# Performance work log

Measured on AMD Instinct MI355X. Metric: run time of the kernel, lower is better.

Reference implementation:

```python
import jax, jax.numpy as jnp
import numpy as np

B = 4; IMG = 32; P = 2; C_IN = 3; H_DIM = 384; DEPTH = 8
GS = IMG // P; L = GS * GS
NSTATE = 16; KDIR = 4; DIN = 384; RANK = 24; MH = int(H_DIM * 4.0)
BOT = 128; NCLS = 1000; TFREQ = 256


def _silu(x):
    return x * jax.nn.sigmoid(x)


def _rms(x, w, eps=1e-6):
    return x * jax.lax.rsqrt(jnp.mean(x * x, -1, keepdims=True) + eps) * w


def _ln(x, w, b, eps=1e-5):
    mu = jnp.mean(x, -1, keepdims=True)
    v = jnp.mean((x - mu) ** 2, -1, keepdims=True)
    return (x - mu) * jax.lax.rsqrt(v + eps) * w + b


def _ln_na(x, eps=1e-6):
    mu = jnp.mean(x, -1, keepdims=True)
    v = jnp.mean((x - mu) ** 2, -1, keepdims=True)
    return (x - mu) * jax.lax.rsqrt(v + eps)


def _mod(x, shift, scale):
    return x * (1.0 + scale[:, None, :]) + shift[:, None, :]


def _ss2d(xin, in_w, conv_w, conv_b, xproj_w, dt_w, dt_b, A_logs, Ds, onorm_w, onorm_b, outp_w):
    Bb = xin.shape[0]
    z = xin @ in_w.T  # (B,L,DIN)
    z2d = z.reshape(Bb, GS, GS, DIN).transpose(0, 3, 1, 2)  # (B,DIN,H,W)
    z2d = jax.lax.conv_general_dilated(z2d, conv_w, (1, 1), 'SAME',
        feature_group_count=DIN, dimension_numbers=('NCHW', 'OIHW', 'NCHW'))
    z2d = _silu(z2d + conv_b[None, :, None, None])
    # cross_scan -> (B,K,DIN,L): row-major, reversed, col-major, reversed col-major
    s1 = z2d.reshape(Bb, DIN, L)
    s3 = z2d.transpose(0, 1, 3, 2).reshape(Bb, DIN, L)
    xs = jnp.stack([s1, s1[..., ::-1], s3, s3[..., ::-1]], axis=1)
    x_dbl = jnp.einsum('bkdl,kod->bkol', xs, xproj_w)
    dtr = x_dbl[:, :, :RANK]
    Bssm = x_dbl[:, :, RANK:RANK + NSTATE]   # (B,K,N,L)
    Cssm = x_dbl[:, :, RANK + NSTATE:]       # (B,K,N,L)
    dt = jnp.einsum('bkrl,kdr->bkdl', dtr, dt_w)
    dt = jax.nn.softplus(dt + dt_b[None, :, :, None])
    A = -jnp.exp(A_logs)                     # (K,DIN,N)
    dA = jnp.exp(jnp.einsum('bkdl,kdn->bkldn', dt, A))
    dBu = jnp.einsum('bkdl,bknl->bkldn', dt * xs, Bssm)
    def comb(e1, e2):
        a1, b1 = e1
        a2, b2 = e2
        return a1 * a2, a2 * b1 + b2
    _, hs = jax.lax.associative_scan(comb, (dA, dBu), axis=2)  # h over token axis
    ys = jnp.einsum('bkldn,bknl->bkdl', hs, Cssm) + Ds[None, :, :, None] * xs
    # cross_merge: undo each direction's reorder and sum
    m1 = ys[:, 0]
    m2 = ys[:, 1][..., ::-1]
    m3 = ys[:, 2].reshape(Bb, DIN, GS, GS).swapaxes(2, 3).reshape(Bb, DIN, L)
    m4 = ys[:, 3][..., ::-1].reshape(Bb, DIN, GS, GS).swapaxes(2, 3).reshape(Bb, DIN, L)
    out = (m1 + m2 + m3 + m4).transpose(0, 2, 1)  # (B,L,DIN)
    out = _ln(out, onorm_w, onorm_b)
    return out @ outp_w.T


def _forward(x, t, y, t_w1, t_b1, t_w2, t_b2, y_table, pe_w1, pe_w2, pe_b2, pos_embed,
             adaln_w, adaln_b, n1_w, n2_w, in_w, conv_w, conv_b, xproj_w, dt_w, dt_b,
             A_logs, Ds, onorm_w, onorm_b, outp_w, mlp_w1, mlp_b1, mlp_w2, mlp_b2,
             f_adaln_w, f_adaln_b, f_lin_w, f_lin_b):
    # timestep embedding (DiT TimestepEmbedder, freq dim 256)
    half = TFREQ // 2
    freqs = jnp.exp(-jnp.log(10000.0) * jnp.arange(half, dtype=jnp.float32) / half)
    ang = t[:, None] * freqs[None]
    temb = jnp.concatenate([jnp.cos(ang), jnp.sin(ang)], axis=-1)
    temb = _silu(temb @ t_w1.T + t_b1) @ t_w2.T + t_b2
    c = temb + y_table[y]  # (B,H_DIM)
    # bottleneck patch embed: patchify -> bottleneck linear -> hidden linear
    xp = x.reshape(B, C_IN, GS, P, GS, P).transpose(0, 2, 4, 1, 3, 5).reshape(B, L, C_IN * P * P)
    h = (xp @ pe_w1.T) @ pe_w2.T + pe_b2
    h = h + pos_embed
    for i in range(DEPTH):
        mod = _silu(c) @ adaln_w[i].T + adaln_b[i]
        sh1, sc1, g1, sh2, sc2, g2 = jnp.split(mod, 6, axis=-1)
        h = h + g1[:, None] * _ss2d(_mod(_rms(h, n1_w[i]), sh1, sc1),
            in_w[i], conv_w[i], conv_b[i], xproj_w[i], dt_w[i], dt_b[i],
            A_logs[i], Ds[i], onorm_w[i], onorm_b[i], outp_w[i])
        u = _mod(_rms(h, n2_w[i]), sh2, sc2)
        u12 = u @ mlp_w1[i].T + mlp_b1[i]
        u1, u2 = jnp.split(u12, 2, axis=-1)
        h = h + g2[:, None] * ((_silu(u1) * u2) @ mlp_w2[i].T + mlp_b2[i])
    modf = _silu(c) @ f_adaln_w.T + f_adaln_b
    shf, scf = jnp.split(modf, 2, axis=-1)
    h = _mod(_ln_na(h), shf, scf)
    out = h @ f_lin_w.T + f_lin_b  # (B,L,P*P*C_IN)
    out = out.reshape(B, GS, GS, P, P, C_IN)
    out = jnp.einsum('nhwpqc->nchpwq', out)
    return out.reshape(B, C_IN, IMG, IMG)


def _sincos_1d(dim, pos):
    omega = 1.0 / (10000.0 ** (np.arange(dim // 2, dtype=np.float64) / (dim / 2.0)))
    out = pos.reshape(-1)[:, None] * omega[None, :]
    return np.concatenate([np.sin(out), np.cos(out)], axis=1)


def _pos_embed_np(dim, gs):
    g = np.stack(np.meshgrid(np.arange(gs, dtype=np.float64), np.arange(gs, dtype=np.float64)), axis=0)
    return np.concatenate([_sincos_1d(dim // 2, g[0]), _sincos_1d(dim // 2, g[1])], axis=1).astype(np.float32)


def setup_inputs():
    key = jax.random.key(0)
    ks = iter(jax.random.split(key, 64))
    nrm = lambda shape, s=0.02: jax.random.normal(next(ks), shape, jnp.float32) * s
    d = {}
    d['x'] = jax.random.normal(next(ks), (B, C_IN, IMG, IMG), jnp.float32)
    d['t'] = jax.random.uniform(next(ks), (B,), jnp.float32) * 1000.0
    d['y'] = jax.random.randint(next(ks), (B,), 0, NCLS)
    d['t_w1'] = nrm((H_DIM, TFREQ)); d['t_b1'] = jnp.zeros((H_DIM,), jnp.float32)
    d['t_w2'] = nrm((H_DIM, H_DIM)); d['t_b2'] = jnp.zeros((H_DIM,), jnp.float32)
    d['y_table'] = nrm((NCLS, H_DIM))
    d['pe_w1'] = nrm((BOT, C_IN * P * P), 0.1)
    d['pe_w2'] = nrm((H_DIM, BOT), 0.1); d['pe_b2'] = jnp.zeros((H_DIM,), jnp.float32)
    d['pos_embed'] = jnp.asarray(_pos_embed_np(H_DIM, GS))[None]
    d['adaln_w'] = nrm((DEPTH, 6 * H_DIM, H_DIM)); d['adaln_b'] = jnp.zeros((DEPTH, 6 * H_DIM), jnp.float32)
    d['n1_w'] = jnp.ones((DEPTH, H_DIM), jnp.float32); d['n2_w'] = jnp.ones((DEPTH, H_DIM), jnp.float32)
    d['in_w'] = nrm((DEPTH, DIN, H_DIM), 0.05)
    d['conv_w'] = nrm((DEPTH, DIN, 1, 3, 3), 0.1); d['conv_b'] = jnp.zeros((DEPTH, DIN), jnp.float32)
    d['xproj_w'] = nrm((DEPTH, KDIR, RANK + 2 * NSTATE, DIN), 0.05)
    d['dt_w'] = nrm((DEPTH, KDIR, DIN, RANK), 0.1)
    d['dt_b'] = nrm((DEPTH, KDIR, DIN), 0.5)
    d['A_logs'] = jnp.tile(jnp.log(jnp.arange(1, NSTATE + 1, dtype=jnp.float32))[None, None, None, :], (DEPTH, KDIR, DIN, 1))
    d['Ds'] = jnp.ones((DEPTH, KDIR, DIN), jnp.float32)
    d['onorm_w'] = jnp.ones((DEPTH, DIN), jnp.float32); d['onorm_b'] = jnp.zeros((DEPTH, DIN), jnp.float32)
    d['outp_w'] = nrm((DEPTH, H_DIM, DIN), 0.05)
    d['mlp_w1'] = nrm((DEPTH, 2 * MH, H_DIM)); d['mlp_b1'] = jnp.zeros((DEPTH, 2 * MH), jnp.float32)
    d['mlp_w2'] = nrm((DEPTH, H_DIM, MH)); d['mlp_b2'] = jnp.zeros((DEPTH, H_DIM), jnp.float32)
    d['f_adaln_w'] = nrm((2 * H_DIM, H_DIM)); d['f_adaln_b'] = jnp.zeros((2 * H_DIM,), jnp.float32)
    d['f_lin_w'] = nrm((P * P * C_IN, H_DIM)); d['f_lin_b'] = jnp.zeros((P * P * C_IN,), jnp.float32)
    return d


def reference(x, t, y, t_w1, t_b1, t_w2, t_b2, y_table, pe_w1, pe_w2, pe_b2, pos_embed,
              adaln_w, adaln_b, n1_w, n2_w, in_w, conv_w, conv_b, xproj_w, dt_w, dt_b,
              A_logs, Ds, onorm_w, onorm_b, outp_w, mlp_w1, mlp_b1, mlp_w2, mlp_b2,
              f_adaln_w, f_adaln_b, f_lin_w, f_lin_b):
    return _forward(x, t, y, t_w1, t_b1, t_w2, t_b2, y_table, pe_w1, pe_w2, pe_b2, pos_embed,
                    adaln_w, adaln_b, n1_w, n2_w, in_w, conv_w, conv_b, xproj_w, dt_w, dt_b,
                    A_logs, Ds, onorm_w, onorm_b, outp_w, mlp_w1, mlp_b1, mlp_w2, mlp_b2,
                    f_adaln_w, f_adaln_b, f_lin_w, f_lin_b)
```

## Files before the change

### kernel.cpp

```cpp
#include <hip/hip_runtime.h>
#include <hip/hip_bf16.h>
#include <math.h>


#define DEV __device__ __forceinline__

typedef __bf16 bf16_t;
typedef __attribute__((ext_vector_type(8))) __bf16 bf16x8;
typedef __attribute__((ext_vector_type(4))) float f32x4;
typedef __attribute__((ext_vector_type(2))) _Float16 h2;

DEV float siluf(float x){ return x / (1.f + __expf(-x)); }
DEV float softplusf(float x){ return fmaxf(x, 0.f) + __logf(1.f + __expf(-fabsf(x))); }

DEV int perm_idx(int k, int l){
  switch(k & 3){
    case 0: return l;
    case 1: return 255 - l;
    case 2: return ((l & 15) << 4) | (l >> 4);
    default: { int r = 255 - l; return ((r & 15) << 4) | (r >> 4); }
  }
}

DEV void cvt_one(int idx, const float* inw, const float* outw, const float* w1,
                 const float* w2, const float* xp, bf16_t* dst){
  const float* src; int off;
  if (idx < 147456){ src = inw;  off = idx; }
  else if (idx < 294912){ src = outw; off = idx - 147456; }
  else if (idx < 1474560){
    int o = idx - 294912;
    int rowc = o / 384, col = o - rowc*384;
    int q = rowc >> 5, tt = rowc & 31;
    int srow = (tt < 16) ? (q*16 + tt) : (1536 + q*16 + (tt - 16));
    src = w1; off = srow*384 + col;
  }
  else if (idx < 2064384){ src = w2; off = idx - 1474560; }
  else { src = xp; off = idx - 2064384; }
  float4 v = *(const float4*)(src + off);
  union { bf16_t h[4]; uint2 u; } cv;
  cv.h[0] = (bf16_t)v.x; cv.h[1] = (bf16_t)v.y; cv.h[2] = (bf16_t)v.z; cv.h[3] = (bf16_t)v.w;
  *(uint2*)(dst + idx) = cv.u;
}

__global__ void k_cvt_layer(const float* __restrict__ inw, const float* __restrict__ outw,
                            const float* __restrict__ w1, const float* __restrict__ w2,
                            const float* __restrict__ xp, bf16_t* __restrict__ dst){
  int idx = (blockIdx.x*256 + threadIdx.x)*4;
  cvt_one(idx, inw, outw, w1, w2, xp, dst);
}

__global__ void k_cvt_all(const float* __restrict__ inw, const float* __restrict__ outw,
                          const float* __restrict__ w1, const float* __restrict__ w2,
                          const float* __restrict__ xp, bf16_t* __restrict__ dst){
  int layer = blockIdx.x / 2100;
  int within = blockIdx.x % 2100;
  int idx = (within*256 + threadIdx.x)*4;
  cvt_one(idx, inw + (size_t)layer*147456, outw + (size_t)layer*147456,
          w1 + (size_t)layer*1179648, w2 + (size_t)layer*589824,
          xp + (size_t)layer*86016, dst + (size_t)layer*2150400);
}

__global__ void k_cond(const float* __restrict__ t, const int* __restrict__ y,
                       const float* __restrict__ tw1, const float* __restrict__ tb1,
                       const float* __restrict__ tw2, const float* __restrict__ tb2,
                       const float* __restrict__ ytab, float* __restrict__ sc){
  int b = blockIdx.x; int o = threadIdx.x;
  __shared__ float temb[256]; __shared__ float h1[384];
  float tv = t[b];
  if (o < 128){
    float f = __expf(-logf(10000.f) * (float)o / 128.f);
    float a = tv * f;
    temb[o] = cosf(a); temb[128 + o] = sinf(a);
  }
  __syncthreads();
  float acc = tb1[o];
  for (int j = 0; j < 256; j++) acc += temb[j] * tw1[(size_t)o*256 + j];
  h1[o] = siluf(acc);
  __syncthreads();
  float acc2 = tb2[o];
  for (int j = 0; j < 384; j++) acc2 += h1[j] * tw2[(size_t)o*384 + j];
  float c = acc2 + ytab[(size_t)y[b]*384 + o];
  sc[b*384 + o] = siluf(c);
}

__global__ void k_patch(const float* __restrict__ x, const float* __restrict__ pw1,
                        const float* __restrict__ pw2, const float* __restrict__ pb2,
                        const float* __restrict__ pos, float* __restrict__ h){
  int bl = blockIdx.x; int b = bl >> 8; int l = bl & 255;
  int gh = l >> 4, gw = l & 15;
  __shared__ float xp[12]; __shared__ float tmp[128];
  int tid = threadIdx.x;
  if (tid < 12){
    int ci = tid >> 2, ph = (tid >> 1) & 1, pw = tid & 1;
    xp[tid] = x[((size_t)(b*3 + ci)*32 + gh*2 + ph)*32 + gw*2 + pw];
  }
  __syncthreads();
  if (tid < 128){
    float a = 0.f;
    #pragma unroll
    for (int k = 0; k < 12; k++) a += xp[k] * pw1[tid*12 + k];
    tmp[tid] = a;
  }
  __syncthreads();
  float a = pb2[tid];
  for (int j = 0; j < 128; j++) a += tmp[j] * pw2[(size_t)tid*128 + j];
  h[(size_t)(b*256 + l)*384 + tid] = a + pos[(size_t)l*384 + tid];
}

__global__ void k_lin_small(const float* __restrict__ sc, const float* __restrict__ W,
                            const float* __restrict__ bias, float* __restrict__ out, int N){
  int idx = blockIdx.x * blockDim.x + threadIdx.x;
  if (idx >= 4*N) return;
  int b = idx / N, o = idx % N;
  const float4* cp = (const float4*)(sc + b*384);
  const float4* wp = (const float4*)(W + (size_t)o*384);
  float a = bias[o];
  #pragma unroll 4
  for (int k = 0; k < 96; k++){
    float4 c4 = cp[k], w4 = wp[k];
    a += c4.x*w4.x + c4.y*w4.y + c4.z*w4.z + c4.w*w4.w;
  }
  out[idx] = a;
}

__global__ void k_rms_mod(const float* __restrict__ h, const float* __restrict__ nw,
                          const float* __restrict__ modBase, bf16_t* __restrict__ out){
  int bl = blockIdx.x; int b = bl >> 8;
  const float* hp = h + (size_t)bl*384;
  const float* mp = modBase + (size_t)b*18432;
  __shared__ float red[2];
  int tid = threadIdx.x;
  float v[3]; float ss = 0.f;
  #pragma unroll
  for (int ii = 0; ii < 3; ii++){ v[ii] = hp[tid + ii*128]; ss += v[ii]*v[ii]; }
  #pragma unroll
  for (int off = 32; off; off >>= 1) ss += __shfl_down(ss, off);
  if ((tid & 63) == 0) red[tid >> 6] = ss;
  __syncthreads();
  ss = red[0] + red[1];
  float inv = rsqrtf(ss / 384.f + 1e-6f);
  #pragma unroll
  for (int ii = 0; ii < 3; ii++){
    int d = tid + ii*128;
    float xv = v[ii] * inv * nw[d];
    out[(size_t)bl*384 + d] = (bf16_t)(xv * (1.f + mp[384 + d]) + mp[d]);
  }
}

template<int MODE>
__global__ __launch_bounds__(256) void k_gemm_bf(
    const bf16_t* __restrict__ A, const bf16_t* __restrict__ W,
    const float* __restrict__ bias, float* __restrict__ C,
    const float* __restrict__ modBase, int N, int K, int Nstore){
  __shared__ bf16_t As[2][64*40];
  __shared__ bf16_t Ws[2][64*40];
  const int tid = threadIdx.x;
  const int bm = blockIdx.y * 64, bn = blockIdx.x * 64;
  const int wave = tid >> 6, lane = tid & 63;
  const int m16 = lane & 15, kg = lane >> 4;
  const int r = tid >> 2, seg = tid & 3;
  const int nt = K / 32;

  uint4 aP, wP;
  auto loadT = [&](int kt){
    wP = *(const uint4*)(W + (size_t)(bn + r)*K + kt*32 + seg*8);
    aP = *(const uint4*)(A + (size_t)(bm + r)*K + kt*32 + seg*8);
  };
  auto stash = [&](int buf){
    *(uint4*)&As[buf][r*40 + seg*8] = aP;
    *(uint4*)&Ws[buf][r*40 + seg*8] = wP;
  };

  f32x4 acc[4] = {};
  loadT(0); stash(0); __syncthreads();
  for (int kt = 0; kt < nt; kt++){
    int buf = kt & 1;
    if (kt + 1 < nt) loadT(kt + 1);
    bf16x8 af = *(bf16x8*)&As[buf][(wave*16 + m16)*40 + kg*8];
    #pragma unroll
    for (int j = 0; j < 4; j++){
      bf16x8 bfr = *(bf16x8*)&Ws[buf][(j*16 + m16)*40 + kg*8];
      acc[j] = __builtin_amdgcn_mfma_f32_16x16x32_bf16(af, bfr, acc[j], 0, 0, 0);
    }
    if (kt + 1 < nt) stash(buf ^ 1);
    __syncthreads();
  }

  if constexpr (MODE == 4){
    bf16_t* Cb = (bf16_t*)C;
    const int Np = N >> 1;
    #pragma unroll
    for (int jp = 0; jp < 2; jp++){
      int pcol = (bn >> 1) + jp*16 + m16;
      float b1v = bias[pcol], b2v = bias[Np + pcol];
      #pragma unroll
      for (int rg = 0; rg < 4; rg++){
        int row = bm + wave*16 + kg*4 + rg;
        float u1v = acc[jp*2][rg] + b1v;
        float u2v = acc[jp*2 + 1][rg] + b2v;
        Cb[(size_t)row*Np + pcol] = (bf16_t)(siluf(u1v)*u2v);
      }
    }
  } else {
    #pragma unroll
    for (int j = 0; j < 4; j++){
      int col = bn + j*16 + m16;
      if (col < Nstore){
        #pragma unroll
        for (int rg = 0; rg < 4; rg++){
          int row = bm + wave*16 + kg*4 + rg;
          float v = acc[j][rg];
          if constexpr (MODE == 5) v += bias[col];
          if constexpr (MODE == 2 || MODE == 5)
            C[(size_t)row*N + col] += modBase[(size_t)(row >> 8)*18432 + col] * v;
          else
            C[(size_t)row*N + col] = v;
        }
      }
    }
  }
}

__global__ void k_conv(const float* __restrict__ z, const float* __restrict__ cw,
                       const float* __restrict__ cb, float* __restrict__ convT,
                       bf16_t* __restrict__ convB){
  int bl = blockIdx.x; int b = bl >> 8, l = bl & 255;
  int hh = l >> 4, ww = l & 15;
  int d = threadIdx.x;
  float acc = cb[d];
  #pragma unroll
  for (int kh = 0; kh < 3; kh++){
    int yy = hh + kh - 1; if ((unsigned)yy > 15u) continue;
    #pragma unroll
    for (int kw = 0; kw < 3; kw++){
      int xx = ww + kw - 1; if ((unsigned)xx > 15u) continue;
      acc += z[(size_t)(b*256 + yy*16 + xx)*384 + d] * cw[d*9 + kh*3 + kw];
    }
  }
  float s = siluf(acc);
  convT[(size_t)bl*384 + d] = s;
  convB[(size_t)bl*384 + d] = (bf16_t)s;
}

__global__ __launch_bounds__(256) void k_scan(
    const float* __restrict__ xdblS, const float* __restrict__ convT,
    const float* __restrict__ dtw, const float* __restrict__ dtb,
    const float* __restrict__ Alog, const float* __restrict__ Dsw,
    float* __restrict__ ysT){
  int blk = blockIdx.x;
  int dp = blk % 192; int k = (blk / 192) & 3; int b = blk / 768;
  int d0 = dp*2;
  int tid = threadIdx.x;
  int n = tid & 15, chunk = tid >> 4;
  __shared__ float sdt[2][256], sxv[2][256], sy[2][256];
  __shared__ float sA[2][16][17], sBc[2][16][17], sPre[2][16][17];
  __shared__ _Float16 sB16[256*18];
  __shared__ _Float16 sC16[256*18];

  {
    int l = tid;
    int lp = perm_idx(k, l);
    const float* row = xdblS + (size_t)(b*256 + lp)*224 + k*56;
    const float4* xr = (const float4*)(row);
    float4 x0 = xr[0], x1 = xr[1], x2 = xr[2], x3 = xr[3], x4 = xr[4], x5 = xr[5];
    #pragma unroll
    for (int j = 0; j < 2; j++){
      const float4* w = (const float4*)(dtw + ((size_t)k*384 + d0 + j)*24);
      float4 w0 = w[0], w1 = w[1], w2 = w[2], w3 = w[3], w4 = w[4], w5 = w[5];
      float a0 = dtb[k*384 + d0 + j];
      a0 += x0.x*w0.x + x0.y*w0.y + x0.z*w0.z + x0.w*w0.w;
      a0 += x1.x*w1.x + x1.y*w1.y + x1.z*w1.z + x1.w*w1.w;
      a0 += x2.x*w2.x + x2.y*w2.y + x2.z*w2.z + x2.w*w2.w;
      a0 += x3.x*w3.x + x3.y*w3.y + x3.z*w3.z + x3.w*w3.w;
      a0 += x4.x*w4.x + x4.y*w4.y + x4.z*w4.z + x4.w*w4.w;
      a0 += x5.x*w5.x + x5.y*w5.y + x5.z*w5.z + x5.w*w5.w;
      sdt[j][l] = softplusf(a0);
    }
    float2 xv2 = *(const float2*)(convT + (size_t)(b*256 + lp)*384 + d0);
    sxv[0][l] = xv2.x; sxv[1][l] = xv2.y;
    const float4* bp = (const float4*)(row + 24);
    h2* bl = (h2*)(sB16 + l*18);
    h2* cl = (h2*)(sC16 + l*18);
    #pragma unroll
    for (int q = 0; q < 4; q++){
      float4 bv = bp[q];
      h2 p0; p0[0] = (_Float16)bv.x; p0[1] = (_Float16)bv.y;
      h2 p1; p1[0] = (_Float16)bv.z; p1[1] = (_Float16)bv.w;
      bl[q*2] = p0; bl[q*2+1] = p1;
      float4 cv = bp[q+4];
      h2 q0; q0[0] = (_Float16)cv.x; q0[1] = (_Float16)cv.y;
      h2 q1; q1[0] = (_Float16)cv.z; q1[1] = (_Float16)cv.w;
      cl[q*2] = q0; cl[q*2+1] = q1;
    }
  }
  __syncthreads();

  float av[2], Dv[2];
  #pragma unroll
  for (int j = 0; j < 2; j++){
    av[j] = -__expf(Alog[((size_t)(k*384) + d0 + j)*16 + n]);
    Dv[j] = Dsw[k*384 + d0 + j];
  }

  float dA[2][16], dBu[2][16];
  float Ap[2] = {1.f, 1.f}, hl[2] = {0.f, 0.f};
  #pragma unroll
  for (int i = 0; i < 16; i++){
    int l = chunk*16 + i;
    float bn16 = (float)sB16[l*18 + n];
    #pragma unroll
    for (int j = 0; j < 2; j++){
      float dtv = sdt[j][l];
      float e = __expf(dtv * av[j]);
      float u = dtv * sxv[j][l] * bn16;
      dA[j][i] = e; dBu[j][i] = u;
      Ap[j] *= e; hl[j] = e*hl[j] + u;
    }
  }
  #pragma unroll
  for (int j = 0; j < 2; j++){ sA[j][chunk][n] = Ap[j]; sBc[j][chunk][n] = hl[j]; }
  __syncthreads();

  if (tid < 32){
    int j = tid >> 4, nn = tid & 15;
    float carry = 0.f;
    #pragma unroll
    for (int c = 0; c < 16; c++){
      sPre[j][c][nn] = carry;
      carry = sA[j][c][nn]*carry + sBc[j][c][nn];
    }
  }
  __syncthreads();

  float hh[2] = {sPre[0][chunk][n], sPre[1][chunk][n]};
  #pragma unroll
  for (int i = 0; i < 16; i++){
    int l = chunk*16 + i;
    float cn = (float)sC16[l*18 + n];
    hh[0] = dA[0][i]*hh[0] + dBu[0][i];
    hh[1] = dA[1][i]*hh[1] + dBu[1][i];
    float p0 = hh[0]*cn, p1 = hh[1]*cn;
    p0 += __shfl_xor(p0, 1); p1 += __shfl_xor(p1, 1);
    p0 += __shfl_xor(p0, 2); p1 += __shfl_xor(p1, 2);
    p0 += __shfl_xor(p0, 4); p1 += __shfl_xor(p1, 4);
    p0 += __shfl_xor(p0, 8); p1 += __shfl_xor(p1, 8);
    if (n == 0){
      sy[0][l] = p0 + Dv[0]*sxv[0][l];
      sy[1][l] = p1 + Dv[1]*sxv[1][l];
    }
  }
  __syncthreads();
  ysT[((size_t)(b*4 + k)*384 + d0)*256 + tid] = sy[0][tid];
  ysT[((size_t)(b*4 + k)*384 + d0 + 1)*256 + tid] = sy[1][tid];
}

__global__ void k_merge_ln(const float* __restrict__ ysT, const float* __restrict__ ow,
                           const float* __restrict__ ob, bf16_t* __restrict__ out){
  int bl = blockIdx.x; int b = bl >> 8; int l = bl & 255;
  int tl = ((l & 15) << 4) | (l >> 4);
  int i2 = 255 - l, i4 = 255 - tl;
  __shared__ float red[4];
  int tid = threadIdx.x;
  const float* base = ysT + (size_t)b*4*384*256;
  float v[3]; float s = 0.f, s2 = 0.f;
  #pragma unroll
  for (int ii = 0; ii < 3; ii++){
    int d = tid + ii*128;
    float vv = base[(size_t)d*256 + l]
             + base[(size_t)(384 + d)*256 + i2]
             + base[(size_t)(768 + d)*256 + tl]
             + base[(size_t)(1152 + d)*256 + i4];
    v[ii] = vv; s += vv; s2 += vv*vv;
  }
  #pragma unroll
  for (int off = 32; off; off >>= 1){ s += __shfl_down(s, off); s2 += __shfl_down(s2, off); }
  if ((tid & 63) == 0){ red[tid >> 6] = s; red[2 + (tid >> 6)] = s2; }
  __syncthreads();
  s = red[0] + red[1]; s2 = red[2] + red[3];
  float mu = s / 384.f;
  float var = s2 / 384.f - mu*mu;
  float inv = rsqrtf(var + 1e-5f);
  #pragma unroll
  for (int ii = 0; ii < 3; ii++){
    int d = tid + ii*128;
    out[(size_t)bl*384 + d] = (bf16_t)((v[ii] - mu) * inv * ow[d] + ob[d]);
  }
}

__global__ void k_final(const float* __restrict__ h, const float* __restrict__ modf,
                        const float* __restrict__ flw, const float* __restrict__ flb,
                        float* __restrict__ out){
  int bl = blockIdx.x; int b = bl >> 8; int l = bl & 255;
  int tid = threadIdx.x;
  __shared__ float buf[384]; __shared__ float red[4];
  const float* hp = h + (size_t)bl*384;
  float v[3]; float s = 0.f, s2 = 0.f;
  #pragma unroll
  for (int ii = 0; ii < 3; ii++){ float xv = hp[tid + ii*128]; v[ii] = xv; s += xv; s2 += xv*xv; }
  #pragma unroll
  for (int off = 32; off; off >>= 1){ s += __shfl_down(s, off); s2 += __shfl_down(s2, off); }
  if ((tid & 63) == 0){ red[tid >> 6] = s; red[2 + (tid >> 6)] = s2; }
  __syncthreads();
  s = red[0] + red[1]; s2 = red[2] + red[3];
  float mu = s / 384.f;
  float var = s2 / 384.f - mu*mu;
  float inv = rsqrtf(var + 1e-6f);
  #pragma unroll
  for (int ii = 0; ii < 3; ii++){
    int d = tid + ii*128;
    buf[d] = (v[ii] - mu) * inv * (1.f + modf[b*768 + 384 + d]) + modf[b*768 + d];
  }
  __syncthreads();
  if (tid < 12){
    float a = flb[tid];
    for (int k = 0; k < 384; k++) a += buf[k] * flw[(size_t)tid*384 + k];
    int p = tid / 6, q = (tid / 3) & 1, cc = tid % 3;
    int gh = l >> 4, gw = l & 15;
    out[((size_t)(b*3 + cc)*32 + gh*2 + p)*32 + gw*2 + q] = a;
  }
}

extern "C" void kernel_launch(void* const* d_in, const int* in_sizes, int n_in,
                              void* d_out, int out_size, void* d_ws, size_t ws_size,
                              hipStream_t stream){
  const float* x       = (const float*)d_in[0];
  const float* t       = (const float*)d_in[1];
  const int*   y       = (const int*)  d_in[2];
  const float* t_w1    = (const float*)d_in[3];
  const float* t_b1    = (const float*)d_in[4];
  const float* t_w2    = (const float*)d_in[5];
  const float* t_b2    = (const float*)d_in[6];
  const float* y_table = (const float*)d_in[7];
  const float* pe_w1   = (const float*)d_in[8];
  const float* pe_w2   = (const float*)d_in[9];
  const float* pe_b2   = (const float*)d_in[10];
  const float* pos     = (const float*)d_in[11];
  const float* adaln_w = (const float*)d_in[12];
  const float* adaln_b = (const float*)d_in[13];
  const float* n1_w    = (const float*)d_in[14];
  const float* n2_w    = (const float*)d_in[15];
  const float* in_w    = (const float*)d_in[16];
  const float* conv_w  = (const float*)d_in[17];
  const float* conv_b  = (const float*)d_in[18];
  const float* xproj_w = (const float*)d_in[19];
  const float* dt_w    = (const float*)d_in[20];
  const float* dt_b    = (const float*)d_in[21];
  const float* A_logs  = (const float*)d_in[22];
  const float* Ds      = (const float*)d_in[23];
  const float* onorm_w = (const float*)d_in[24];
  const float* onorm_b = (const float*)d_in[25];
  const float* outp_w  = (const float*)d_in[26];
  const float* mlp_w1  = (const float*)d_in[27];
  const float* mlp_b1  = (const float*)d_in[28];
  const float* mlp_w2  = (const float*)d_in[29];
  const float* mlp_b2  = (const float*)d_in[30];
  const float* f_adaln_w = (const float*)d_in[31];
  const float* f_adaln_b = (const float*)d_in[32];
  const float* f_lin_w = (const float*)d_in[33];
  const float* f_lin_b = (const float*)d_in[34];

  float* ws = (float*)d_ws;
  float*  sc      = ws + 0;
  float*  h       = ws + 1536;
  float*  modAll  = ws + 394752;
  float*  modf    = ws + 468480;
  float*  buf1    = ws + 471552;
  float*  convT   = ws + 864768;
  float*  xdblS   = ws + 1257984;
  bf16_t* u12b    = (bf16_t*)(ws + 1487360);
  float*  ysT     = ws + 2273792;
  bf16_t* xin_bf  = (bf16_t*)(ws + 3846656);
  bf16_t* ssin_bf = (bf16_t*)(ws + 4043264);
  bf16_t* conv_bf = (bf16_t*)(ws + 4239872);
  bf16_t* wbfBase = (bf16_t*)(ws + 4436480);

  const bool bigws = ws_size >= (size_t)13038080 * 4;

  k_cond<<<dim3(4), dim3(384), 0, stream>>>(t, y, t_w1, t_b1, t_w2, t_b2, y_table, sc);
  k_patch<<<dim3(1024), dim3(384), 0, stream>>>(x, pe_w1, pe_w2, pe_b2, pos, h);
  k_lin_small<<<dim3(288), dim3(256), 0, stream>>>(sc, adaln_w, adaln_b, modAll, 18432);
  if (bigws)
    k_cvt_all<<<dim3(16800), dim3(256), 0, stream>>>(
        in_w, outp_w, mlp_w1, mlp_w2, xproj_w, wbfBase);

  for (int i = 0; i < 8; i++){
    const float* modL = modAll + (size_t)i*2304;
    bf16_t* wbf = bigws ? wbfBase + (size_t)i*2150400 : wbfBase;
    if (!bigws)
      k_cvt_layer<<<dim3(2100), dim3(256), 0, stream>>>(
          in_w + (size_t)i*147456, outp_w + (size_t)i*147456, mlp_w1 + (size_t)i*1179648,
          mlp_w2 + (size_t)i*589824, xproj_w + (size_t)i*86016, wbf);
    bf16_t* wbf_in  = wbf;
    bf16_t* wbf_out = wbf + 147456;
    bf16_t* wbf_w1  = wbf + 294912;
    bf16_t* wbf_w2  = wbf + 1474560;
    bf16_t* wbf_xp  = wbf + 2064384;

    k_rms_mod<<<dim3(1024), dim3(128), 0, stream>>>(h, n1_w + i*384, modL + 0, xin_bf);
    k_gemm_bf<0><<<dim3(6,16), dim3(256), 0, stream>>>(
        xin_bf, wbf_in, nullptr, buf1, nullptr, 384, 384, 384);
    k_conv<<<dim3(1024), dim3(384), 0, stream>>>(
        buf1, conv_w + (size_t)i*384*9, conv_b + i*384, convT, conv_bf);
    k_gemm_bf<0><<<dim3(4,16), dim3(256), 0, stream>>>(
        conv_bf, wbf_xp, nullptr, xdblS, nullptr, 224, 384, 224);
    k_scan<<<dim3(3072), dim3(256), 0, stream>>>(
        xdblS, convT, dt_w + (size_t)i*4*384*24, dt_b + (size_t)i*4*384,
        A_logs + (size_t)i*4*384*16, Ds + (size_t)i*4*384, ysT);
    k_merge_ln<<<dim3(1024), dim3(128), 0, stream>>>(
        ysT, onorm_w + i*384, onorm_b + i*384, ssin_bf);
    k_gemm_bf<2><<<dim3(6,16), dim3(256), 0, stream>>>(
        ssin_bf, wbf_out, nullptr, h, modL + 768, 384, 384, 384);
    k_rms_mod<<<dim3(1024), dim3(128), 0, stream>>>(h, n2_w + i*384, modL + 1152, xin_bf);
    k_gemm_bf<4><<<dim3(48,16), dim3(256), 0, stream>>>(
        xin_bf, wbf_w1, mlp_b1 + (size_t)i*3072, (float*)u12b, nullptr, 3072, 384, 3072);
    k_gemm_bf<5><<<dim3(6,16), dim3(256), 0, stream>>>(
        u12b, wbf_w2, mlp_b2 + (size_t)i*384, h, modL + 1920, 384, 1536, 384);
  }

  k_lin_small<<<dim3(12), dim3(256), 0, stream>>>(sc, f_adaln_w, f_adaln_b, modf, 768);
  k_final<<<dim3(1024), dim3(128), 0, stream>>>(h, modf, f_lin_w, f_lin_b, (float*)d_out);
}
```

Before: 1.177 ms.

## Process four channels per scan block and split conditioning MLP across more blocks

```diff
diff --git a/kernel.cpp b/kernel.cpp
--- a/kernel.cpp
+++ b/kernel.cpp
@@ -60,26 +60,50 @@
           xp + (size_t)layer*86016, dst + (size_t)layer*2150400);
 }
 
-__global__ void k_cond(const float* __restrict__ t, const int* __restrict__ y,
-                       const float* __restrict__ tw1, const float* __restrict__ tb1,
-                       const float* __restrict__ tw2, const float* __restrict__ tb2,
-                       const float* __restrict__ ytab, float* __restrict__ sc){
-  int b = blockIdx.x; int o = threadIdx.x;
-  __shared__ float temb[256]; __shared__ float h1[384];
+__global__ void k_cond1(const float* __restrict__ t, const float* __restrict__ tw1,
+                        const float* __restrict__ tb1, float* __restrict__ h1g){
+  int b = blockIdx.x / 3, ch = blockIdx.x % 3;
+  int tid = threadIdx.x;
+  int o = ch*128 + tid;
+  __shared__ float temb[256];
   float tv = t[b];
-  if (o < 128){
-    float f = __expf(-logf(10000.f) * (float)o / 128.f);
+  {
+    float f = __expf(-logf(10000.f) * (float)tid / 128.f);
     float a = tv * f;
-    temb[o] = cosf(a); temb[128 + o] = sinf(a);
-  }
-  __syncthreads();
+    temb[tid] = cosf(a); temb[128 + tid] = sinf(a);
+  }
+  __syncthreads();
+  const float4* te = (const float4*)temb;
+  const float4* wp = (const float4*)(tw1 + (size_t)o*256);
   float acc = tb1[o];
-  for (int j = 0; j < 256; j++) acc += temb[j] * tw1[(size_t)o*256 + j];
-  h1[o] = siluf(acc);
-  __syncthreads();
-  float acc2 = tb2[o];
-  for (int j = 0; j < 384; j++) acc2 += h1[j] * tw2[(size_t)o*384 + j];
-  float c = acc2 + ytab[(size_t)y[b]*384 + o];
+  #pragma unroll 8
+  for (int j = 0; j < 64; j++){
+    float4 c4 = te[j], w4 = wp[j];
+    acc += c4.x*w4.x + c4.y*w4.y + c4.z*w4.z + c4.w*w4.w;
+  }
+  h1g[b*384 + o] = siluf(acc);
+}
+
+__global__ void k_cond2(const int* __restrict__ y, const float* __restrict__ h1g,
+                        const float* __restrict__ tw2, const float* __restrict__ tb2,
+                        const float* __restrict__ ytab, float* __restrict__ sc){
+  int b = blockIdx.x / 3, ch = blockIdx.x % 3;
+  int tid = threadIdx.x;
+  int o = ch*128 + tid;
+  __shared__ float h1[384];
+  h1[tid] = h1g[b*384 + tid];
+  h1[tid + 128] = h1g[b*384 + tid + 128];
+  h1[tid + 256] = h1g[b*384 + tid + 256];
+  __syncthreads();
+  const float4* hp = (const float4*)h1;
+  const float4* wp = (const float4*)(tw2 + (size_t)o*384);
+  float acc = tb2[o];
+  #pragma unroll 8
+  for (int j = 0; j < 96; j++){
+    float4 c4 = hp[j], w4 = wp[j];
+    acc += c4.x*w4.x + c4.y*w4.y + c4.z*w4.z + c4.w*w4.w;
+  }
+  float c = acc + ytab[(size_t)y[b]*384 + o];
   sc[b*384 + o] = siluf(c);
 }
 
@@ -248,12 +272,12 @@
     const float* __restrict__ Alog, const float* __restrict__ Dsw,
     float* __restrict__ ysT){
   int blk = blockIdx.x;
-  int dp = blk % 192; int k = (blk / 192) & 3; int b = blk / 768;
-  int d0 = dp*2;
+  int dq = blk % 96; int k = (blk / 96) & 3; int b = blk / 384;
+  int d0 = dq*4;
   int tid = threadIdx.x;
   int n = tid & 15, chunk = tid >> 4;
-  __shared__ float sdt[2][256], sxv[2][256], sy[2][256];
-  __shared__ float sA[2][16][17], sBc[2][16][17], sPre[2][16][17];
+  __shared__ float sdt[4][256], sxv[4][256], sy[4][256];
+  __shared__ float sA[4][16][17], sBc[4][16][17], sPre[4][16][17];
   __shared__ _Float16 sB16[256*18];
   __shared__ _Float16 sC16[256*18];
 
@@ -264,7 +288,7 @@
     const float4* xr = (const float4*)(row);
     float4 x0 = xr[0], x1 = xr[1], x2 = xr[2], x3 = xr[3], x4 = xr[4], x5 = xr[5];
     #pragma unroll
-    for (int j = 0; j < 2; j++){
+    for (int j = 0; j < 4; j++){
       const float4* w = (const float4*)(dtw + ((size_t)k*384 + d0 + j)*24);
       float4 w0 = w[0], w1 = w[1], w2 = w[2], w3 = w[3], w4 = w[4], w5 = w[5];
       float a0 = dtb[k*384 + d0 + j];
@@ -276,8 +300,8 @@
       a0 += x5.x*w5.x + x5.y*w5.y + x5.z*w5.z + x5.w*w5.w;
       sdt[j][l] = softplusf(a0);
     }
-    float2 xv2 = *(const float2*)(convT + (size_t)(b*256 + lp)*384 + d0);
-    sxv[0][l] = xv2.x; sxv[1][l] = xv2.y;
+    float4 xv4 = *(const float4*)(convT + (size_t)(b*256 + lp)*384 + d0);
+    sxv[0][l] = xv4.x; sxv[1][l] = xv4.y; sxv[2][l] = xv4.z; sxv[3][l] = xv4.w;
     const float4* bp = (const float4*)(row + 24);
     h2* bl = (h2*)(sB16 + l*18);
     h2* cl = (h2*)(sC16 + l*18);
@@ -295,21 +319,21 @@
   }
   __syncthreads();
 
-  float av[2], Dv[2];
-  #pragma unroll
-  for (int j = 0; j < 2; j++){
+  float av[4], Dv[4];
+  #pragma unroll
+  for (int j = 0; j < 4; j++){
     av[j] = -__expf(Alog[((size_t)(k*384) + d0 + j)*16 + n]);
     Dv[j] = Dsw[k*384 + d0 + j];
   }
 
-  float dA[2][16], dBu[2][16];
-  float Ap[2] = {1.f, 1.f}, hl[2] = {0.f, 0.f};
+  float dA[4][16], dBu[4][16];
+  float Ap[4] = {1.f, 1.f, 1.f, 1.f}, hl[4] = {0.f, 0.f, 0.f, 0.f};
   #pragma unroll
   for (int i = 0; i < 16; i++){
     int l = chunk*16 + i;
     float bn16 = (float)sB16[l*18 + n];
     #pragma unroll
-    for (int j = 0; j < 2; j++){
+    for (int j = 0; j < 4; j++){
       float dtv = sdt[j][l];
       float e = __expf(dtv * av[j]);
       float u = dtv * sxv[j][l] * bn16;
@@ -318,10 +342,10 @@
     }
   }
   #pragma unroll
-  for (int j = 0; j < 2; j++){ sA[j][chunk][n] = Ap[j]; sBc[j][chunk][n] = hl[j]; }
-  __syncthreads();
-
-  if (tid < 32){
+  for (int j = 0; j < 4; j++){ sA[j][chunk][n] = Ap[j]; sBc[j][chunk][n] = hl[j]; }
+  __syncthreads();
+
+  if (tid < 64){
     int j = tid >> 4, nn = tid & 15;
     float carry = 0.f;
     #pragma unroll
@@ -332,26 +356,28 @@
   }
   __syncthreads();
 
-  float hh[2] = {sPre[0][chunk][n], sPre[1][chunk][n]};
+  float hh[4];
+  #pragma unroll
+  for (int j = 0; j < 4; j++) hh[j] = sPre[j][chunk][n];
   #pragma unroll
   for (int i = 0; i < 16; i++){
     int l = chunk*16 + i;
     float cn = (float)sC16[l*18 + n];
-    hh[0] = dA[0][i]*hh[0] + dBu[0][i];
-    hh[1] = dA[1][i]*hh[1] + dBu[1][i];
-    float p0 = hh[0]*cn, p1 = hh[1]*cn;
-    p0 += __shfl_xor(p0, 1); p1 += __shfl_xor(p1, 1);
-    p0 += __shfl_xor(p0, 2); p1 += __shfl_xor(p1, 2);
-    p0 += __shfl_xor(p0, 4); p1 += __shfl_xor(p1, 4);
-    p0 += __shfl_xor(p0, 8); p1 += __shfl_xor(p1, 8);
-    if (n == 0){
-      sy[0][l] = p0 + Dv[0]*sxv[0][l];
-      sy[1][l] = p1 + Dv[1]*sxv[1][l];
-    }
-  }
-  __syncthreads();
-  ysT[((size_t)(b*4 + k)*384 + d0)*256 + tid] = sy[0][tid];
-  ysT[((size_t)(b*4 + k)*384 + d0 + 1)*256 + tid] = sy[1][tid];
+    #pragma unroll
+    for (int j = 0; j < 4; j++){
+      hh[j] = dA[j][i]*hh[j] + dBu[j][i];
+      float p = hh[j]*cn;
+      p += __shfl_xor(p, 1);
+      p += __shfl_xor(p, 2);
+      p += __shfl_xor(p, 4);
+      p += __shfl_xor(p, 8);
+      if (n == 0) sy[j][l] = p + Dv[j]*sxv[j][l];
+    }
+  }
+  __syncthreads();
+  #pragma unroll
+  for (int j = 0; j < 4; j++)
+    ysT[((size_t)(b*4 + k)*384 + d0 + j)*256 + tid] = sy[j][tid];
 }
 
 __global__ void k_merge_ln(const float* __restrict__ ysT, const float* __restrict__ ow,
@@ -473,10 +499,12 @@
   bf16_t* ssin_bf = (bf16_t*)(ws + 4043264);
   bf16_t* conv_bf = (bf16_t*)(ws + 4239872);
   bf16_t* wbfBase = (bf16_t*)(ws + 4436480);
+  float*  h1g     = ysT;
 
   const bool bigws = ws_size >= (size_t)13038080 * 4;
 
-  k_cond<<<dim3(4), dim3(384), 0, stream>>>(t, y, t_w1, t_b1, t_w2, t_b2, y_table, sc);
+  k_cond1<<<dim3(12), dim3(128), 0, stream>>>(t, t_w1, t_b1, h1g);
+  k_cond2<<<dim3(12), dim3(128), 0, stream>>>(y, h1g, t_w2, t_b2, y_table, sc);
   k_patch<<<dim3(1024), dim3(384), 0, stream>>>(x, pe_w1, pe_w2, pe_b2, pos, h);
   k_lin_small<<<dim3(288), dim3(256), 0, stream>>>(sc, adaln_w, adaln_b, modAll, 18432);
   if (bigws)
@@ -503,7 +531,7 @@
         buf1, conv_w + (size_t)i*384*9, conv_b + i*384, convT, conv_bf);
     k_gemm_bf<0><<<dim3(4,16), dim3(256), 0, stream>>>(
         conv_bf, wbf_xp, nullptr, xdblS, nullptr, 224, 384, 224);
-    k_scan<<<dim3(3072), dim3(256), 0, stream>>>(
+    k_scan<<<dim3(1536), dim3(256), 0, stream>>>(
         xdblS, convT, dt_w + (size_t)i*4*384*24, dt_b + (size_t)i*4*384,
         A_logs + (size_t)i*4*384*16, Ds + (size_t)i*4*384, ysT);
     k_merge_ln<<<dim3(1024), dim3(128), 0, stream>>>(
```

Result: slower. 1.283 ms (+9.0%).
